# Kernel tuning notes

Measured on AMD Instinct MI355X. Metric: run time of the kernel, lower is better.

Reference implementation:

```python
import jax, jax.numpy as jnp
import numpy as np

B, N, IN_F = 16, 1024, 256
HEADS, OUT_F = 4, 64
NEG_SLOPE = 0.2
CLAMP_MIN = -1e9
MASK_VAL = -9e15


def setup_inputs() -> dict:
    key = jax.random.key(0)
    k1, k2, k3, k4 = jax.random.split(key, 4)
    x = jax.random.normal(k1, (B, N, IN_F), dtype=jnp.float32)
    adj = jax.random.randint(k2, (B, N, N), 0, 2, dtype=jnp.int32)
    # Linear weight, stored as (in, heads*out) so y = x @ W (xavier-uniform scale)
    lim_w = float(np.sqrt(6.0 / (IN_F + HEADS * OUT_F)))
    W = jax.random.uniform(k3, (IN_F, HEADS * OUT_F), dtype=jnp.float32,
                           minval=-lim_w, maxval=lim_w)
    lim_a = float(np.sqrt(6.0 / (2 * OUT_F + HEADS)))
    a = jax.random.uniform(k4, (2 * OUT_F, HEADS), dtype=jnp.float32,
                           minval=-lim_a, maxval=lim_a)
    return {"x": x, "adj": adj, "W": W, "a": a}


def reference(x, adj, W, a):
    Bs, Ns, _ = x.shape
    # Projection: (B,N,H,D)
    h = (x @ W).reshape(Bs, Ns, HEADS, OUT_F)
    # cat([h_i, h_j]) . a == h_i . a_src + h_j . a_dst  (exact same math, no O(N^2*2D) tensor)
    a_src, a_dst = a[:OUT_F], a[OUT_F:]          # each (D, H)
    s_src = jnp.einsum('bnhd,dh->bnh', h, a_src)  # score contribution of node i
    s_dst = jnp.einsum('bnhd,dh->bnh', h, a_dst)  # score contribution of node j
    e = jax.nn.leaky_relu(s_src[:, :, None, :] + s_dst[:, None, :, :],
                          negative_slope=NEG_SLOPE)  # (B,N,N,H)
    # match original: subtract unmasked row max, clamp, then mask, then softmax over j
    e = e - jnp.max(e, axis=2, keepdims=True)
    e = jnp.maximum(e, CLAMP_MIN)
    att = jnp.where(adj[..., None] > 0, e, MASK_VAL)
    att = jax.nn.softmax(att, axis=2)
    h_prime = jnp.einsum('bijh,bjhd->bihd', att, h)  # (B,N,H,D)
    return h_prime.reshape(Bs, Ns, HEADS * OUT_F)
```

## Files before the change

### kernel.cpp

```cpp
#include <hip/hip_runtime.h>
#include <hip/hip_bf16.h>

#define B_   16
#define N_   1024
#define INF_ 256
#define NH_  4
#define HD_  256
#define L2E  1.4426950408889634f

typedef __attribute__((ext_vector_type(8))) short short8;
typedef __attribute__((ext_vector_type(4))) float f32x4;

__device__ __forceinline__ float bf2f(unsigned short u) {
    union { unsigned int i; float f; } v; v.i = ((unsigned int)u) << 16; return v.f;
}
__device__ __forceinline__ unsigned short f2bf(float f) {
    union { float f; unsigned int i; } v; v.f = f;
    unsigned int x = v.i;
    return (unsigned short)((x + 0x7fffu + ((x >> 16) & 1u)) >> 16);
}
__device__ __forceinline__ unsigned int cvt_pk_bf16(float lo, float hi) {
    unsigned int r;
    asm("v_cvt_pk_bf16_f32 %0, %1, %2" : "=v"(r) : "v"(lo), "v"(hi));
    return r;
}

__global__ __launch_bounds__(256) void k_prep(const int* __restrict__ adj,
                                              const float* __restrict__ W,
                                              unsigned int* __restrict__ pb,
                                              unsigned short* __restrict__ wswz)
{
    int bx = blockIdx.x, t = threadIdx.x;
    if (bx < 2048) {
        int wave = t >> 6, lane = t & 63;
        int row = bx * 8 + wave * 2 + (lane >> 5);
        int w   = lane & 31;
        const int4* ar = (const int4*)(adj + ((long)row << 10) + w * 32);
        unsigned int u = 0;
        #pragma unroll
        for (int k = 0; k < 8; k++) {
            int4 a = ar[k];
            u |= ((unsigned)a.x) << (4 * k);
            u |= ((unsigned)a.y) << (4 * k + 1);
            u |= ((unsigned)a.z) << (4 * k + 2);
            u |= ((unsigned)a.w) << (4 * k + 3);
        }
        pb[((long)row << 5) + w] = u;
    } else {
        int slot = (bx - 2048) * 256 + t;
        int kstep = slot >> 10;
        int nt    = (slot >> 6) & 15;
        int lane  = slot & 63;
        int k0 = kstep * 32 + (lane >> 4) * 8;
        int n  = nt * 16 + (lane & 15);
        ushort4 o0, o1;
        o0.x = f2bf(W[(k0 + 0) * HD_ + n]);
        o0.y = f2bf(W[(k0 + 1) * HD_ + n]);
        o0.z = f2bf(W[(k0 + 2) * HD_ + n]);
        o0.w = f2bf(W[(k0 + 3) * HD_ + n]);
        o1.x = f2bf(W[(k0 + 4) * HD_ + n]);
        o1.y = f2bf(W[(k0 + 5) * HD_ + n]);
        o1.z = f2bf(W[(k0 + 6) * HD_ + n]);
        o1.w = f2bf(W[(k0 + 7) * HD_ + n]);
        *(ushort4*)&wswz[(long)slot * 8]     = o0;
        *(ushort4*)&wswz[(long)slot * 8 + 4] = o1;
    }
}

__global__ __launch_bounds__(256) void k_gemm_h(
    const float* __restrict__ x, const float* __restrict__ a,
    const unsigned short* __restrict__ wswz,
    unsigned short* __restrict__ hswz,
    float2* __restrict__ esrc, float2* __restrict__ edst)
{
    __shared__ unsigned short xls[16][264];
    int t = threadIdx.x;
    int blk = blockIdx.x;
    int row0 = blk * 16;
    int b  = blk >> 6;
    int n0 = row0 & 1023;

    {
        int sr = t >> 4, sc = (t & 15) * 16;
        const float* xp = x + (long)(row0 + sr) * INF_ + sc;
        float4 v0 = ((const float4*)xp)[0];
        float4 v1 = ((const float4*)xp)[1];
        float4 v2 = ((const float4*)xp)[2];
        float4 v3 = ((const float4*)xp)[3];
        ushort4 u0 = {f2bf(v0.x), f2bf(v0.y), f2bf(v0.z), f2bf(v0.w)};
        ushort4 u1 = {f2bf(v1.x), f2bf(v1.y), f2bf(v1.z), f2bf(v1.w)};
        ushort4 u2 = {f2bf(v2.x), f2bf(v2.y), f2bf(v2.z), f2bf(v2.w)};
        ushort4 u3 = {f2bf(v3.x), f2bf(v3.y), f2bf(v3.z), f2bf(v3.w)};
        *(ushort4*)&xls[sr][sc]      = u0;
        *(ushort4*)&xls[sr][sc + 4]  = u1;
        *(ushort4*)&xls[sr][sc + 8]  = u2;
        *(ushort4*)&xls[sr][sc + 12] = u3;
    }
    __syncthreads();

    int wave = t >> 6, lane = t & 63, quad = lane >> 4, l15 = lane & 15;
    f32x4 acc[4];
    #pragma unroll
    for (int i = 0; i < 4; i++) acc[i] = (f32x4){0.f, 0.f, 0.f, 0.f};

    #pragma unroll
    for (int ks = 0; ks < 8; ks++) {
        short8 af = *(const short8*)&xls[l15][ks * 32 + quad * 8];
        #pragma unroll
        for (int nt = 0; nt < 4; nt++) {
            short8 bf = *(const short8*)(wswz +
                ((long)((ks * 16 + wave * 4 + nt) * 64 + lane)) * 8);
            acc[nt] = __builtin_amdgcn_mfma_f32_16x16x32_bf16(af, bf, acc[nt], 0, 0, 0);
        }
    }

    int q0 = (quad & 1) * 4;
    int qd = ((row0 & 31) + quad * 4) >> 3;
    long bj32 = row0 >> 5;
    #pragma unroll
    for (int nt = 0; nt < 4; nt++) {
        int dg = wave * 4 + nt;
        long idx8 = (bj32 * 16 + dg) * 64 + qd * 16 + l15;
        ushort4 o = {f2bf(acc[nt][0]), f2bf(acc[nt][1]),
                     f2bf(acc[nt][2]), f2bf(acc[nt][3])};
        *(ushort4*)&hswz[idx8 * 8 + q0] = o;
    }

    float as_[4], ad_[4];
    #pragma unroll
    for (int nt = 0; nt < 4; nt++) {
        int d = nt * 16 + l15;
        as_[nt] = a[d * NH_ + wave];
        ad_[nt] = a[(64 + d) * NH_ + wave];
    }
    #pragma unroll
    for (int r = 0; r < 4; r++) {
        float ps = acc[0][r] * as_[0] + acc[1][r] * as_[1]
                 + acc[2][r] * as_[2] + acc[3][r] * as_[3];
        float pd = acc[0][r] * ad_[0] + acc[1][r] * ad_[1]
                 + acc[2][r] * ad_[2] + acc[3][r] * ad_[3];
        #pragma unroll
        for (int m = 1; m < 16; m <<= 1) {
            ps += __shfl_xor(ps, m);
            pd += __shfl_xor(pd, m);
        }
        if (l15 == 0) {
            int row = n0 + quad * 4 + r;
            float s1 = ps * L2E, s2 = pd * L2E;
            esrc[((long)b * NH_ + wave) * N_ + row] =
                make_float2(__builtin_exp2f(s1), __builtin_exp2f(0.2f * s1));
            edst[((long)b * NH_ + wave) * N_ + row] =
                make_float2(__builtin_exp2f(s2), __builtin_exp2f(0.2f * s2));
        }
    }
}

__global__ __launch_bounds__(512, 4) void k_attn(
    const unsigned int* __restrict__ pb, const unsigned short* __restrict__ hswz,
    const float2* __restrict__ esrc, const float2* __restrict__ edst,
    float* __restrict__ out)
{
    __shared__ float2 es_s[4][32];
    __shared__ uint2 mtab[16];
    __shared__ float accb[4][2][64][20];

    int t = threadIdx.x;
    int b  = blockIdx.x >> 5, ig = blockIdx.x & 31;
    int i0 = ig * 32;
    int wave = t >> 6, lane = t & 63, quad = lane >> 4, l15 = lane & 15;
    int hh = wave & 3, jh = wave >> 2;

    if (t < 128) {
        int h = t >> 5, i = t & 31;
        es_s[h][i] = esrc[((long)(b * NH_ + h)) * N_ + i0 + i];
    }
    if (t >= 128 && t < 144) {
        int k = t - 128;
        unsigned int w0 = ((k & 1) ? 0xffffu : 0u) | ((k & 2) ? 0xffff0000u : 0u);
        unsigned int w1 = ((k & 4) ? 0xffffu : 0u) | ((k & 8) ? 0xffff0000u : 0u);
        mtab[k] = make_uint2(w0, w1);
    }
    __syncthreads();

    float2 es0 = es_s[hh][l15];
    float2 es1 = es_s[hh][16 + l15];
    const float2* edp = edst + ((long)(b * NH_ + hh)) * N_ + jh * 512;
    long grow0 = ((long)b << 10) + i0 + l15;
    const unsigned int* pb0 = pb + (grow0 << 5) + jh * 16;
    const unsigned int* pb1 = pb0 + (16 << 5);

    f32x4 acc0[4], acc1[4], dn0, dn1;
    #pragma unroll
    for (int i = 0; i < 4; i++) {
        acc0[i] = (f32x4){0.f, 0.f, 0.f, 0.f};
        acc1[i] = (f32x4){0.f, 0.f, 0.f, 0.f};
    }
    dn0 = (f32x4){0.f, 0.f, 0.f, 0.f};
    dn1 = (f32x4){0.f, 0.f, 0.f, 0.f};
    short8 ones;
    #pragma unroll
    for (int i = 0; i < 8; i++) ones[i] = (short)0x3F80;

    int shq = quad * 8;

    #pragma unroll 4
    for (int jc = 0; jc < 16; jc++) {
        unsigned int m0 = (pb0[jc] >> shq) & 0xffu;
        unsigned int m1 = (pb1[jc] >> shq) & 0xffu;
        const float4* ej = (const float4*)(edp + jc * 32 + quad * 8);

        union { unsigned int u[4]; short8 s; } p0, p1;
        #pragma unroll
        for (int qp = 0; qp < 4; qp++) {
            float4 d = ej[qp];
            float lo0 = fmaxf(es0.x * d.x, es0.y * d.y);
            float hi0 = fmaxf(es0.x * d.z, es0.y * d.w);
            float lo1 = fmaxf(es1.x * d.x, es1.y * d.y);
            float hi1 = fmaxf(es1.x * d.z, es1.y * d.w);
            p0.u[qp] = cvt_pk_bf16(lo0, hi0);
            p1.u[qp] = cvt_pk_bf16(lo1, hi1);
        }
        uint2 ma0 = mtab[m0 & 15u], mb0 = mtab[m0 >> 4];
        uint2 ma1 = mtab[m1 & 15u], mb1 = mtab[m1 >> 4];
        p0.u[0] &= ma0.x; p0.u[1] &= ma0.y; p0.u[2] &= mb0.x; p0.u[3] &= mb0.y;
        p1.u[0] &= ma1.x; p1.u[1] &= ma1.y; p1.u[2] &= mb1.x; p1.u[3] &= mb1.y;

        long s8 = ((long)(b * 32 + jh * 16 + jc)) * 1024;
        #pragma unroll
        for (int idt = 0; idt < 4; idt++) {
            short8 bf = *(const short8*)(hswz + (s8 + (hh * 4 + idt) * 64 + lane) * 8);
            acc0[idt] = __builtin_amdgcn_mfma_f32_16x16x32_bf16(p0.s, bf, acc0[idt], 0, 0, 0);
            acc1[idt] = __builtin_amdgcn_mfma_f32_16x16x32_bf16(p1.s, bf, acc1[idt], 0, 0, 0);
        }
        dn0 = __builtin_amdgcn_mfma_f32_16x16x32_bf16(p0.s, ones, dn0, 0, 0, 0);
        dn1 = __builtin_amdgcn_mfma_f32_16x16x32_bf16(p1.s, ones, dn1, 0, 0, 0);
    }

    if (jh == 1) {
        #pragma unroll
        for (int idt = 0; idt < 4; idt++) {
            *(f32x4*)&accb[hh][0][lane][idt * 4] = acc0[idt];
            *(f32x4*)&accb[hh][1][lane][idt * 4] = acc1[idt];
        }
        *(f32x4*)&accb[hh][0][lane][16] = dn0;
        *(f32x4*)&accb[hh][1][lane][16] = dn1;
    }
    __syncthreads();

    if (jh == 0) {
        f32x4 od0 = *(const f32x4*)&accb[hh][0][lane][16];
        f32x4 od1 = *(const f32x4*)&accb[hh][1][lane][16];
        float inv0[4], inv1[4];
        #pragma unroll
        for (int r = 0; r < 4; r++) {
            inv0[r] = 1.0f / (dn0[r] + od0[r]);
            inv1[r] = 1.0f / (dn1[r] + od1[r]);
        }
        #pragma unroll
        for (int idt = 0; idt < 4; idt++) {
            f32x4 o0 = *(const f32x4*)&accb[hh][0][lane][idt * 4];
            f32x4 o1 = *(const f32x4*)&accb[hh][1][lane][idt * 4];
            int col = hh * 64 + idt * 16 + l15;
            #pragma unroll
            for (int r = 0; r < 4; r++) {
                long row_g = (long)b * N_ + i0 + quad * 4 + r;
                out[row_g * HD_ + col] = (acc0[idt][r] + o0[r]) * inv0[r];
                out[(row_g + 16) * HD_ + col] = (acc1[idt][r] + o1[r]) * inv1[r];
            }
        }
    }
}

extern "C" void kernel_launch(void* const* d_in, const int* in_sizes, int n_in,
                              void* d_out, int out_size, void* d_ws, size_t ws_size,
                              hipStream_t stream) {
    const float* x   = (const float*)d_in[0];
    const int*   adj = (const int*)d_in[1];
    const float* W   = (const float*)d_in[2];
    const float* a   = (const float*)d_in[3];
    float* out = (float*)d_out;

    unsigned int* pb      = (unsigned int*)d_ws;
    unsigned short* hswz  = (unsigned short*)(pb + 524288);
    unsigned short* wswz  = hswz + (long)B_ * N_ * HD_;
    float2* esrc = (float2*)(wswz + INF_ * HD_);
    float2* edst = esrc + (long)B_ * NH_ * N_;

    k_prep<<<2080, 256, 0, stream>>>(adj, W, pb, wswz);
    k_gemm_h<<<1024, 256, 0, stream>>>(x, a, wswz, hswz, esrc, edst);
    k_attn<<<512, 512, 0, stream>>>(pb, hswz, esrc, edst, out);
}
```

Before: 155.0 us.

## Halve attention row tile and fold source exponent into per-row ratio

```diff
diff --git a/kernel.cpp b/kernel.cpp
--- a/kernel.cpp
+++ b/kernel.cpp
@@ -71,7 +71,7 @@
     const float* __restrict__ x, const float* __restrict__ a,
     const unsigned short* __restrict__ wswz,
     unsigned short* __restrict__ hswz,
-    float2* __restrict__ esrc, float2* __restrict__ edst)
+    float* __restrict__ esr, float2* __restrict__ edst)
 {
     __shared__ unsigned short xls[16][264];
     int t = threadIdx.x;
@@ -147,56 +147,44 @@
         if (l15 == 0) {
             int row = n0 + quad * 4 + r;
             float s1 = ps * L2E, s2 = pd * L2E;
-            esrc[((long)b * NH_ + wave) * N_ + row] =
-                make_float2(__builtin_exp2f(s1), __builtin_exp2f(0.2f * s1));
+            esr[((long)b * NH_ + wave) * N_ + row] = __builtin_exp2f(-0.8f * s1);
             edst[((long)b * NH_ + wave) * N_ + row] =
                 make_float2(__builtin_exp2f(s2), __builtin_exp2f(0.2f * s2));
         }
     }
 }
 
-__global__ __launch_bounds__(512, 4) void k_attn(
+__global__ __launch_bounds__(512, 8) void k_attn(
     const unsigned int* __restrict__ pb, const unsigned short* __restrict__ hswz,
-    const float2* __restrict__ esrc, const float2* __restrict__ edst,
+    const float* __restrict__ esr, const float2* __restrict__ edst,
     float* __restrict__ out)
 {
-    __shared__ float2 es_s[4][32];
     __shared__ uint2 mtab[16];
-    __shared__ float accb[4][2][64][20];
+    __shared__ float accb[4][64][20];
 
     int t = threadIdx.x;
-    int b  = blockIdx.x >> 5, ig = blockIdx.x & 31;
-    int i0 = ig * 32;
+    int b  = blockIdx.x >> 6, ig = blockIdx.x & 63;
+    int i0 = ig * 16;
     int wave = t >> 6, lane = t & 63, quad = lane >> 4, l15 = lane & 15;
     int hh = wave & 3, jh = wave >> 2;
 
-    if (t < 128) {
-        int h = t >> 5, i = t & 31;
-        es_s[h][i] = esrc[((long)(b * NH_ + h)) * N_ + i0 + i];
-    }
-    if (t >= 128 && t < 144) {
-        int k = t - 128;
+    if (t < 16) {
+        int k = t;
         unsigned int w0 = ((k & 1) ? 0xffffu : 0u) | ((k & 2) ? 0xffff0000u : 0u);
         unsigned int w1 = ((k & 4) ? 0xffffu : 0u) | ((k & 8) ? 0xffff0000u : 0u);
         mtab[k] = make_uint2(w0, w1);
     }
     __syncthreads();
 
-    float2 es0 = es_s[hh][l15];
-    float2 es1 = es_s[hh][16 + l15];
+    float r0 = esr[((long)(b * NH_ + hh)) * N_ + i0 + l15];
     const float2* edp = edst + ((long)(b * NH_ + hh)) * N_ + jh * 512;
     long grow0 = ((long)b << 10) + i0 + l15;
     const unsigned int* pb0 = pb + (grow0 << 5) + jh * 16;
-    const unsigned int* pb1 = pb0 + (16 << 5);
-
-    f32x4 acc0[4], acc1[4], dn0, dn1;
-    #pragma unroll
-    for (int i = 0; i < 4; i++) {
-        acc0[i] = (f32x4){0.f, 0.f, 0.f, 0.f};
-        acc1[i] = (f32x4){0.f, 0.f, 0.f, 0.f};
-    }
-    dn0 = (f32x4){0.f, 0.f, 0.f, 0.f};
-    dn1 = (f32x4){0.f, 0.f, 0.f, 0.f};
+
+    f32x4 acc[4], dn;
+    #pragma unroll
+    for (int i = 0; i < 4; i++) acc[i] = (f32x4){0.f, 0.f, 0.f, 0.f};
+    dn = (f32x4){0.f, 0.f, 0.f, 0.f};
     short8 ones;
     #pragma unroll
     for (int i = 0; i < 8; i++) ones[i] = (short)0x3F80;
@@ -206,66 +194,49 @@
     #pragma unroll 4
     for (int jc = 0; jc < 16; jc++) {
         unsigned int m0 = (pb0[jc] >> shq) & 0xffu;
-        unsigned int m1 = (pb1[jc] >> shq) & 0xffu;
         const float4* ej = (const float4*)(edp + jc * 32 + quad * 8);
 
-        union { unsigned int u[4]; short8 s; } p0, p1;
+        union { unsigned int u[4]; short8 s; } p0;
         #pragma unroll
         for (int qp = 0; qp < 4; qp++) {
             float4 d = ej[qp];
-            float lo0 = fmaxf(es0.x * d.x, es0.y * d.y);
-            float hi0 = fmaxf(es0.x * d.z, es0.y * d.w);
-            float lo1 = fmaxf(es1.x * d.x, es1.y * d.y);
-            float hi1 = fmaxf(es1.x * d.z, es1.y * d.w);
-            p0.u[qp] = cvt_pk_bf16(lo0, hi0);
-            p1.u[qp] = cvt_pk_bf16(lo1, hi1);
-        }
-        uint2 ma0 = mtab[m0 & 15u], mb0 = mtab[m0 >> 4];
-        uint2 ma1 = mtab[m1 & 15u], mb1 = mtab[m1 >> 4];
-        p0.u[0] &= ma0.x; p0.u[1] &= ma0.y; p0.u[2] &= mb0.x; p0.u[3] &= mb0.y;
-        p1.u[0] &= ma1.x; p1.u[1] &= ma1.y; p1.u[2] &= mb1.x; p1.u[3] &= mb1.y;
+            float lo = fmaxf(d.x, r0 * d.y);
+            float hi = fmaxf(d.z, r0 * d.w);
+            p0.u[qp] = cvt_pk_bf16(lo, hi);
+        }
+        uint2 ma = mtab[m0 & 15u], mb = mtab[m0 >> 4];
+        p0.u[0] &= ma.x; p0.u[1] &= ma.y; p0.u[2] &= mb.x; p0.u[3] &= mb.y;
 
         long s8 = ((long)(b * 32 + jh * 16 + jc)) * 1024;
         #pragma unroll
         for (int idt = 0; idt < 4; idt++) {
             short8 bf = *(const short8*)(hswz + (s8 + (hh * 4 + idt) * 64 + lane) * 8);
-            acc0[idt] = __builtin_amdgcn_mfma_f32_16x16x32_bf16(p0.s, bf, acc0[idt], 0, 0, 0);
-            acc1[idt] = __builtin_amdgcn_mfma_f32_16x16x32_bf16(p1.s, bf, acc1[idt], 0, 0, 0);
-        }
-        dn0 = __builtin_amdgcn_mfma_f32_16x16x32_bf16(p0.s, ones, dn0, 0, 0, 0);
-        dn1 = __builtin_amdgcn_mfma_f32_16x16x32_bf16(p1.s, ones, dn1, 0, 0, 0);
+            acc[idt] = __builtin_amdgcn_mfma_f32_16x16x32_bf16(p0.s, bf, acc[idt], 0, 0, 0);
+        }
+        dn = __builtin_amdgcn_mfma_f32_16x16x32_bf16(p0.s, ones, dn, 0, 0, 0);
     }
 
     if (jh == 1) {
         #pragma unroll
+        for (int idt = 0; idt < 4; idt++)
+            *(f32x4*)&accb[hh][lane][idt * 4] = acc[idt];
+        *(f32x4*)&accb[hh][lane][16] = dn;
+    }
+    __syncthreads();
+
+    if (jh == 0) {
+        f32x4 od = *(const f32x4*)&accb[hh][lane][16];
+        float inv[4];
+        #pragma unroll
+        for (int r = 0; r < 4; r++) inv[r] = 1.0f / (dn[r] + od[r]);
+        #pragma unroll
         for (int idt = 0; idt < 4; idt++) {
-            *(f32x4*)&accb[hh][0][lane][idt * 4] = acc0[idt];
-            *(f32x4*)&accb[hh][1][lane][idt * 4] = acc1[idt];
-        }
-        *(f32x4*)&accb[hh][0][lane][16] = dn0;
-        *(f32x4*)&accb[hh][1][lane][16] = dn1;
-    }
-    __syncthreads();
-
-    if (jh == 0) {
-        f32x4 od0 = *(const f32x4*)&accb[hh][0][lane][16];
-        f32x4 od1 = *(const f32x4*)&accb[hh][1][lane][16];
-        float inv0[4], inv1[4];
-        #pragma unroll
-        for (int r = 0; r < 4; r++) {
-            inv0[r] = 1.0f / (dn0[r] + od0[r]);
-            inv1[r] = 1.0f / (dn1[r] + od1[r]);
-        }
-        #pragma unroll
-        for (int idt = 0; idt < 4; idt++) {
-            f32x4 o0 = *(const f32x4*)&accb[hh][0][lane][idt * 4];
-            f32x4 o1 = *(const f32x4*)&accb[hh][1][lane][idt * 4];
+            f32x4 o = *(const f32x4*)&accb[hh][lane][idt * 4];
             int col = hh * 64 + idt * 16 + l15;
             #pragma unroll
             for (int r = 0; r < 4; r++) {
                 long row_g = (long)b * N_ + i0 + quad * 4 + r;
-                out[row_g * HD_ + col] = (acc0[idt][r] + o0[r]) * inv0[r];
-                out[(row_g + 16) * HD_ + col] = (acc1[idt][r] + o1[r]) * inv1[r];
+                out[row_g * HD_ + col] = (acc[idt][r] + o[r]) * inv[r];
             }
         }
     }
@@ -283,10 +254,10 @@
     unsigned int* pb      = (unsigned int*)d_ws;
     unsigned short* hswz  = (unsigned short*)(pb + 524288);
     unsigned short* wswz  = hswz + (long)B_ * N_ * HD_;
-    float2* esrc = (float2*)(wswz + INF_ * HD_);
-    float2* edst = esrc + (long)B_ * NH_ * N_;
+    float* esr   = (float*)(wswz + INF_ * HD_);
+    float2* edst = (float2*)(esr + (long)B_ * NH_ * N_);
 
     k_prep<<<2080, 256, 0, stream>>>(adj, W, pb, wswz);
-    k_gemm_h<<<1024, 256, 0, stream>>>(x, a, wswz, hswz, esrc, edst);
-    k_attn<<<512, 512, 0, stream>>>(pb, hswz, esrc, edst, out);
-}
+    k_gemm_h<<<1024, 256, 0, stream>>>(x, a, wswz, hswz, esr, edst);
+    k_attn<<<1024, 512, 0, stream>>>(pb, hswz, esr, edst, out);
+}
```

Result: slower. 165.7 us (+6.9%).

## Fold per-row source exponent into ratio and swizzle attention block order

Applied to the files above, without the earlier changes.

```diff
diff --git a/kernel.cpp b/kernel.cpp
--- a/kernel.cpp
+++ b/kernel.cpp
@@ -71,7 +71,7 @@
     const float* __restrict__ x, const float* __restrict__ a,
     const unsigned short* __restrict__ wswz,
     unsigned short* __restrict__ hswz,
-    float2* __restrict__ esrc, float2* __restrict__ edst)
+    float* __restrict__ esr, float2* __restrict__ edst)
 {
     __shared__ unsigned short xls[16][264];
     int t = threadIdx.x;
@@ -147,8 +147,7 @@
         if (l15 == 0) {
             int row = n0 + quad * 4 + r;
             float s1 = ps * L2E, s2 = pd * L2E;
-            esrc[((long)b * NH_ + wave) * N_ + row] =
-                make_float2(__builtin_exp2f(s1), __builtin_exp2f(0.2f * s1));
+            esr[((long)b * NH_ + wave) * N_ + row] = __builtin_exp2f(-0.8f * s1);
             edst[((long)b * NH_ + wave) * N_ + row] =
                 make_float2(__builtin_exp2f(s2), __builtin_exp2f(0.2f * s2));
         }
@@ -157,33 +156,30 @@
 
 __global__ __launch_bounds__(512, 4) void k_attn(
     const unsigned int* __restrict__ pb, const unsigned short* __restrict__ hswz,
-    const float2* __restrict__ esrc, const float2* __restrict__ edst,
+    const float* __restrict__ esr, const float2* __restrict__ edst,
     float* __restrict__ out)
 {
-    __shared__ float2 es_s[4][32];
     __shared__ uint2 mtab[16];
     __shared__ float accb[4][2][64][20];
 
     int t = threadIdx.x;
-    int b  = blockIdx.x >> 5, ig = blockIdx.x & 31;
+    int bid = blockIdx.x;
+    int swz = (bid & 7) * 64 + (bid >> 3);
+    int b  = swz >> 5, ig = swz & 31;
     int i0 = ig * 32;
     int wave = t >> 6, lane = t & 63, quad = lane >> 4, l15 = lane & 15;
     int hh = wave & 3, jh = wave >> 2;
 
-    if (t < 128) {
-        int h = t >> 5, i = t & 31;
-        es_s[h][i] = esrc[((long)(b * NH_ + h)) * N_ + i0 + i];
-    }
-    if (t >= 128 && t < 144) {
-        int k = t - 128;
+    if (t < 16) {
+        int k = t;
         unsigned int w0 = ((k & 1) ? 0xffffu : 0u) | ((k & 2) ? 0xffff0000u : 0u);
         unsigned int w1 = ((k & 4) ? 0xffffu : 0u) | ((k & 8) ? 0xffff0000u : 0u);
         mtab[k] = make_uint2(w0, w1);
     }
     __syncthreads();
 
-    float2 es0 = es_s[hh][l15];
-    float2 es1 = es_s[hh][16 + l15];
+    float r0 = esr[((long)(b * NH_ + hh)) * N_ + i0 + l15];
+    float r1 = esr[((long)(b * NH_ + hh)) * N_ + i0 + 16 + l15];
     const float2* edp = edst + ((long)(b * NH_ + hh)) * N_ + jh * 512;
     long grow0 = ((long)b << 10) + i0 + l15;
     const unsigned int* pb0 = pb + (grow0 << 5) + jh * 16;
@@ -213,12 +209,8 @@
         #pragma unroll
         for (int qp = 0; qp < 4; qp++) {
             float4 d = ej[qp];
-            float lo0 = fmaxf(es0.x * d.x, es0.y * d.y);
-            float hi0 = fmaxf(es0.x * d.z, es0.y * d.w);
-            float lo1 = fmaxf(es1.x * d.x, es1.y * d.y);
-            float hi1 = fmaxf(es1.x * d.z, es1.y * d.w);
-            p0.u[qp] = cvt_pk_bf16(lo0, hi0);
-            p1.u[qp] = cvt_pk_bf16(lo1, hi1);
+            p0.u[qp] = cvt_pk_bf16(fmaxf(d.x, r0 * d.y), fmaxf(d.z, r0 * d.w));
+            p1.u[qp] = cvt_pk_bf16(fmaxf(d.x, r1 * d.y), fmaxf(d.z, r1 * d.w));
         }
         uint2 ma0 = mtab[m0 & 15u], mb0 = mtab[m0 >> 4];
         uint2 ma1 = mtab[m1 & 15u], mb1 = mtab[m1 >> 4];
@@ -283,10 +275,10 @@
     unsigned int* pb      = (unsigned int*)d_ws;
     unsigned short* hswz  = (unsigned short*)(pb + 524288);
     unsigned short* wswz  = hswz + (long)B_ * N_ * HD_;
-    float2* esrc = (float2*)(wswz + INF_ * HD_);
-    float2* edst = esrc + (long)B_ * NH_ * N_;
+    float* esr   = (float*)(wswz + INF_ * HD_);
+    float2* edst = (float2*)(esr + (long)B_ * NH_ * N_);
 
     k_prep<<<2080, 256, 0, stream>>>(adj, W, pb, wswz);
-    k_gemm_h<<<1024, 256, 0, stream>>>(x, a, wswz, hswz, esrc, edst);
-    k_attn<<<512, 512, 0, stream>>>(pb, hswz, esrc, edst, out);
-}
+    k_gemm_h<<<1024, 256, 0, stream>>>(x, a, wswz, hswz, esr, edst);
+    k_attn<<<512, 512, 0, stream>>>(pb, hswz, esr, edst, out);
+}
```

After: 153.3 us. Within noise of the previous version (-1.1%).
